# Kernel tuning notes

Hardware: AMD Instinct MI355X
Metric: run time of the kernel (lower is better)

Reference implementation:

```python
import jax, jax.numpy as jnp
import numpy as np

L = 32            # num_layers
R = 16            # lora_rank
P = L * 7         # 224 projections
D = 256           # encoder d_model
H = 4             # encoder heads
HD = D // H
FF = 2048         # TransformerEncoderLayer default dim_feedforward
PED = 512         # proj_embed_dim
HID = 4096
KV = 8 * (4096 // 32)   # 1024
INTER = 11008
VOCAB = 50000
NEG = -1e9

# projection index groups within the P=7*L ordering [q,k,v,o,gate,up,down]
IDX_A_HID = jnp.asarray((np.arange(L)[:, None] * 7 + np.array([0, 1, 2, 3, 4, 5])).reshape(-1))  # in_dim=4096
IDX_A_INT = jnp.asarray(np.arange(L) * 7 + 6)                                                    # in_dim=11008
IDX_B_HID = jnp.asarray((np.arange(L)[:, None] * 7 + np.array([0, 3, 6])).reshape(-1))           # out_dim=4096
IDX_B_KV  = jnp.asarray((np.arange(L)[:, None] * 7 + np.array([1, 2])).reshape(-1))              # out_dim=1024
IDX_B_INT = jnp.asarray((np.arange(L)[:, None] * 7 + np.array([4, 5])).reshape(-1))              # out_dim=11008


def _ln(x, g, b, eps=1e-5):
    m = jnp.mean(x, -1, keepdims=True)
    v = jnp.mean((x - m) ** 2, -1, keepdims=True)
    return (x - m) * jax.lax.rsqrt(v + eps) * g + b


def _enc_layer(x, pad, qw, qb, ow, ob, g1, b1, f1w, f1b, f2w, f2b, g2, b2):
    # post-norm TransformerEncoderLayer (torch default), relu FFN, eval mode (no dropout)
    Bsz, S, _ = x.shape
    qkv = x @ qw.T + qb                                  # [B,S,3D]
    q, k, v = jnp.split(qkv, 3, axis=-1)
    hd = lambda t: t.reshape(Bsz, S, H, HD).transpose(0, 2, 1, 3)
    q, k, v = hd(q), hd(k), hd(v)
    s = jnp.einsum('bhqd,bhkd->bhqk', q, k) / jnp.asarray(np.sqrt(HD), x.dtype)
    s = jnp.where(pad[:, None, None, :], NEG, s)
    a = jax.nn.softmax(s, -1)
    o = jnp.einsum('bhqk,bhkd->bhqd', a, v).transpose(0, 2, 1, 3).reshape(Bsz, S, D)
    x = _ln(x + o @ ow.T + ob, g1, b1)
    f = jax.nn.relu(x @ f1w.T + f1b) @ f2w.T + f2b
    return _ln(x + f, g2, b2)


def _forward(condition_ids, attention_mask, embed_table, enc_qkv_w, enc_qkv_b, enc_out_w, enc_out_b,
             enc_ln1_g, enc_ln1_b, enc_ff1_w, enc_ff1_b, enc_ff2_w, enc_ff2_b, enc_ln2_g, enc_ln2_b,
             proj_w, proj_b, a1_w, a1_b, a2_w, a2_b, b1_w, b1_b, b2_w, b2_b, scales):
    Bsz = condition_ids.shape[0]
    x = embed_table[condition_ids]                       # [B,S,256]
    pad = attention_mask == 0                            # key padding mask (~attention_mask)
    for l in range(3):
        x = _enc_layer(x, pad, enc_qkv_w[l], enc_qkv_b[l], enc_out_w[l], enc_out_b[l],
                       enc_ln1_g[l], enc_ln1_b[l], enc_ff1_w[l], enc_ff1_b[l],
                       enc_ff2_w[l], enc_ff2_b[l], enc_ln2_g[l], enc_ln2_b[l])
    am = attention_mask.astype(x.dtype)
    pooled = (x * am[..., None]).sum(1) / jnp.clip(am.sum(1, keepdims=True), 1.0)   # masked mean pool
    pe = (pooled @ proj_w.T + proj_b).reshape(Bsz, P, PED)                          # [B,224,512]

    def dec(w1, b1_, w2, b2_):
        return jax.nn.gelu(pe @ w1.T + b1_, approximate=False) @ w2.T + b2_

    A_base = dec(a1_w, a1_b, a2_w, a2_b).reshape(Bsz, P, R, 64)   # [B,P,r,64]
    B_base = dec(b1_w, b1_b, b2_w, b2_b).reshape(Bsz, P, 64, R)   # [B,P,64,r]
    sa, sb = scales[:, 0], scales[:, 1]

    def tile_A(idx, in_d):
        # all in_dims divisible by 64 => repeat(in_d//64+1)[:, :in_d] == exact tiling
        a = A_base[:, idx] * sa[idx][None, :, None, None]
        return jnp.tile(a, (1, 1, 1, in_d // 64))

    def tile_B(idx, out_d):
        b = B_base[:, idx] * sb[idx][None, :, None, None]
        return jnp.tile(b, (1, 1, out_d // 64, 1))

    return (tile_A(IDX_A_HID, HID), tile_A(IDX_A_INT, INTER),
            tile_B(IDX_B_HID, HID), tile_B(IDX_B_KV, KV), tile_B(IDX_B_INT, INTER))


def setup_inputs() -> dict:
    key = jax.random.key(0)
    ks = iter(jax.random.split(key, 40))
    rn = lambda shape, s=0.02: jax.random.normal(next(ks), shape, jnp.float32) * s
    Bsz, S = 4, 128
    return {
        'condition_ids': jax.random.randint(next(ks), (Bsz, S), 0, VOCAB),
        'attention_mask': jnp.ones((Bsz, S), jnp.int32),
        'embed_table': rn((VOCAB, D)),
        'enc_qkv_w': rn((3, 3 * D, D)), 'enc_qkv_b': rn((3, 3 * D)),
        'enc_out_w': rn((3, D, D)), 'enc_out_b': rn((3, D)),
        'enc_ln1_g': jnp.ones((3, D)), 'enc_ln1_b': jnp.zeros((3, D)),
        'enc_ff1_w': rn((3, FF, D)), 'enc_ff1_b': rn((3, FF)),
        'enc_ff2_w': rn((3, D, FF)), 'enc_ff2_b': rn((3, D)),
        'enc_ln2_g': jnp.ones((3, D)), 'enc_ln2_b': jnp.zeros((3, D)),
        'proj_w': rn((P * PED, D)), 'proj_b': rn((P * PED,)),
        'a1_w': rn((D, PED)), 'a1_b': rn((D,)),
        'a2_w': rn((R * 64, D)), 'a2_b': rn((R * 64,)),
        'b1_w': rn((D, PED)), 'b1_b': rn((D,)),
        'b2_w': rn((R * 64, D)), 'b2_b': rn((R * 64,)),
        'scales': jnp.full((P, 2), 0.01, jnp.float32),
    }


def reference(condition_ids, attention_mask, embed_table, enc_qkv_w, enc_qkv_b, enc_out_w, enc_out_b,
              enc_ln1_g, enc_ln1_b, enc_ff1_w, enc_ff1_b, enc_ff2_w, enc_ff2_b, enc_ln2_g, enc_ln2_b,
              proj_w, proj_b, a1_w, a1_b, a2_w, a2_b, b1_w, b1_b, b2_w, b2_b, scales):
    return _forward(condition_ids, attention_mask, embed_table, enc_qkv_w, enc_qkv_b, enc_out_w, enc_out_b,
                    enc_ln1_g, enc_ln1_b, enc_ff1_w, enc_ff1_b, enc_ff2_w, enc_ff2_b, enc_ln2_g, enc_ln2_b,
                    proj_w, proj_b, a1_w, a1_b, a2_w, a2_b, b1_w, b1_b, b2_w, b2_b, scales)
```

## Files before the change

### kernel.cpp

```cpp
#include <hip/hip_runtime.h>
#include <hip/hip_bf16.h>

typedef unsigned short u16;
typedef unsigned int u32;
typedef __attribute__((ext_vector_type(8))) short short8;
typedef __attribute__((ext_vector_type(4))) float floatx4;

__device__ __forceinline__ u16 f2bf(float f) {
  u32 x = __float_as_uint(f);
  x += 0x7FFFu + ((x >> 16) & 1u);
  return (u16)(x >> 16);
}
__device__ __forceinline__ u32 pk2(float lo, float hi) {
  return (u32)f2bf(lo) | ((u32)f2bf(hi) << 16);
}

__global__ void embed_kernel(const int* __restrict__ ids, const float* __restrict__ emb,
                             float* __restrict__ x) {
  int tok = blockIdx.x, d = threadIdx.x;
  x[tok * 256 + d] = emb[(size_t)ids[tok] * 256 + d];
}

template <int ACT, int SPLIT>
__global__ __launch_bounds__(256) void mfma_gemm_kernel(const float* __restrict__ A,
    const float* __restrict__ W, const float* __restrict__ bias, float* __restrict__ C,
    int M, int N, int K, int KS, int pstride) {
  __shared__ u16 Abf[64 * 32];
  __shared__ u16 Wbf[64 * 32];
  const int t = threadIdx.x;
  const int m0 = blockIdx.x * 64, n0 = blockIdx.y * 64;
  const int kz = blockIdx.z;
  const int srow = t >> 2, skc = (t & 3) * 8;
  const int w = t >> 6, lane = t & 63;
  const int q = lane >> 4, rr = lane & 15;
  floatx4 acc[4];
#pragma unroll
  for (int i = 0; i < 4; ++i) acc[i] = (floatx4){0.f, 0.f, 0.f, 0.f};

  const int kbeg = kz * KS, kend = kbeg + KS;
  for (int k0 = kbeg; k0 < kend; k0 += 32) {
    const float* ga = A + (size_t)(m0 + srow) * K + k0 + skc;
    const float* gw = W + (size_t)(n0 + srow) * K + k0 + skc;
    float4 a0 = *(const float4*)ga;
    float4 a1 = *(const float4*)(ga + 4);
    float4 w0 = *(const float4*)gw;
    float4 w1 = *(const float4*)(gw + 4);
    uint4 pa, pw;
    pa.x = pk2(a0.x, a0.y); pa.y = pk2(a0.z, a0.w);
    pa.z = pk2(a1.x, a1.y); pa.w = pk2(a1.z, a1.w);
    pw.x = pk2(w0.x, w0.y); pw.y = pk2(w0.z, w0.w);
    pw.z = pk2(w1.x, w1.y); pw.w = pk2(w1.z, w1.w);
    __syncthreads();
    *(uint4*)&Abf[srow * 32 + skc] = pa;
    *(uint4*)&Wbf[srow * 32 + skc] = pw;
    __syncthreads();
    short8 af = *(short8*)&Abf[(w * 16 + rr) * 32 + q * 8];
#pragma unroll
    for (int ct = 0; ct < 4; ++ct) {
      short8 bf = *(short8*)&Wbf[(ct * 16 + rr) * 32 + q * 8];
      acc[ct] = __builtin_amdgcn_mfma_f32_16x16x32_bf16(af, bf, acc[ct], 0, 0, 0);
    }
  }

  float* dst = SPLIT ? (C + (size_t)kz * pstride) : C;
#pragma unroll
  for (int ct = 0; ct < 4; ++ct) {
    int col = n0 + ct * 16 + rr;
#pragma unroll
    for (int r = 0; r < 4; ++r) {
      int row = m0 + w * 16 + q * 4 + r;
      float v = acc[ct][r];
      if (!SPLIT) {
        v += bias[col];
        if (ACT == 1) v = fmaxf(v, 0.f);
        if (ACT == 2) v = 0.5f * v * (1.f + erff(v * 0.70710678118654752f));
      }
      dst[(size_t)row * N + col] = v;
    }
  }
}

template <int ACT>
__global__ void red_bias_act_kernel(const float* __restrict__ parts, int nparts, int pstride,
                                    const float* __restrict__ bias, float* __restrict__ dst, int N) {
  int idx = blockIdx.x * 256 + threadIdx.x;
  float v = bias[idx % N];
  for (int p = 0; p < nparts; ++p) v += parts[(size_t)p * pstride + idx];
  if (ACT == 1) v = fmaxf(v, 0.f);
  if (ACT == 2) v = 0.5f * v * (1.f + erff(v * 0.70710678118654752f));
  dst[idx] = v;
}

__global__ __launch_bounds__(256) void attn_kernel(const float* __restrict__ qkv,
    const int* __restrict__ mask, float* __restrict__ o) {
  __shared__ float Klds[8192];
  __shared__ float Vlds[8192];
  const int blk = blockIdx.x;
  const int b = blk >> 7, h = (blk >> 5) & 3, qg = blk & 31;
  const int t = threadIdx.x;
  for (int i = t; i < 8192; i += 256) {
    int s = i >> 6, d = i & 63;
    size_t base = (size_t)(b * 128 + s) * 768 + h * 64 + d;
    Klds[(s << 6) + (d ^ (s & 31))] = qkv[base + 256];
    Vlds[i] = qkv[base + 512];
  }
  __syncthreads();
  const int wave = t >> 6, lane = t & 63;
  const int q = qg * 4 + wave;
  float qv = qkv[(size_t)(b * 128 + q) * 768 + h * 64 + lane];
  const int m0i = mask[b * 128 + lane];
  const int m1i = mask[b * 128 + 64 + lane];
  float s0 = 0.f, s1 = 0.f;
  const int sw = lane & 31;
  for (int d = 0; d < 64; ++d) {
    float qd = __shfl(qv, d);
    s0 += qd * Klds[(lane << 6) + (d ^ sw)];
    s1 += qd * Klds[((lane + 64) << 6) + (d ^ sw)];
  }
  s0 *= 0.125f; s1 *= 0.125f;
  if (m0i == 0) s0 = -1000000000.0f;
  if (m1i == 0) s1 = -1000000000.0f;
  float m = fmaxf(s0, s1);
  for (int off = 32; off; off >>= 1) m = fmaxf(m, __shfl_xor(m, off));
  float p0 = expf(s0 - m), p1 = expf(s1 - m);
  float sum = p0 + p1;
  for (int off = 32; off; off >>= 1) sum += __shfl_xor(sum, off);
  float rs = 1.f / sum;
  float acc = 0.f;
  for (int k = 0; k < 64; ++k) acc += __shfl(p0, k) * Vlds[(k << 6) + lane];
  for (int k = 0; k < 64; ++k) acc += __shfl(p1, k) * Vlds[((k + 64) << 6) + lane];
  o[(size_t)(b * 128 + q) * 256 + h * 64 + lane] = acc * rs;
}

__global__ __launch_bounds__(256) void add_ln_red_kernel(float* __restrict__ x,
    const float* __restrict__ parts, int nparts, int pstride, const float* __restrict__ bias,
    const float* __restrict__ g, const float* __restrict__ b) {
  int tok = blockIdx.x, t = threadIdx.x;
  int idx = tok * 256 + t;
  float r = x[idx] + bias[t];
  for (int p = 0; p < nparts; ++p) r += parts[(size_t)p * pstride + idx];
  float s = r, sq = r * r;
  for (int off = 32; off; off >>= 1) { s += __shfl_xor(s, off); sq += __shfl_xor(sq, off); }
  __shared__ float red[8];
  int wave = t >> 6, lane = t & 63;
  if (lane == 0) { red[wave] = s; red[4 + wave] = sq; }
  __syncthreads();
  float S = red[0] + red[1] + red[2] + red[3];
  float SQ = red[4] + red[5] + red[6] + red[7];
  float mean = S * (1.f / 256.f);
  float var = SQ * (1.f / 256.f) - mean * mean;
  float inv = 1.f / sqrtf(fmaxf(var, 0.f) + 1e-5f);
  x[idx] = (r - mean) * inv * g[t] + b[t];
}

__global__ void pool_kernel(const float* __restrict__ x, const int* __restrict__ mask,
                            float* __restrict__ pooled) {
  int b = blockIdx.x, d = threadIdx.x;
  float s = 0.f, c = 0.f;
  for (int ss = 0; ss < 128; ++ss) {
    float m = (float)mask[b * 128 + ss];
    s += m * x[(size_t)(b * 128 + ss) * 256 + d];
    c += m;
  }
  pooled[b * 256 + d] = s / fmaxf(c, 1.f);
}

__global__ __launch_bounds__(256) void proj_kernel(const float* __restrict__ pooled,
    const float* __restrict__ W, const float* __restrict__ bias, float* __restrict__ pe) {
  __shared__ float pl[1024];
  int t = threadIdx.x;
  for (int i = t; i < 1024; i += 256) pl[i] = pooled[i];
  __syncthreads();
  int wave = t >> 6, lane = t & 63;
  int half = lane >> 5, sl = lane & 31;
  int row = blockIdx.x * 8 + wave * 2 + half;
  float4 w0 = *(const float4*)(W + (size_t)row * 256 + sl * 8);
  float4 w1 = *(const float4*)(W + (size_t)row * 256 + sl * 8 + 4);
  float a0, a1, a2, a3;
#pragma unroll
  for (int bb = 0; bb < 4; ++bb) {
    const float* pp = &pl[bb * 256 + sl * 8];
    float v = w0.x * pp[0] + w0.y * pp[1] + w0.z * pp[2] + w0.w * pp[3]
            + w1.x * pp[4] + w1.y * pp[5] + w1.z * pp[6] + w1.w * pp[7];
    if (bb == 0) a0 = v; else if (bb == 1) a1 = v; else if (bb == 2) a2 = v; else a3 = v;
  }
#pragma unroll
  for (int off = 1; off < 32; off <<= 1) {
    a0 += __shfl_xor(a0, off); a1 += __shfl_xor(a1, off);
    a2 += __shfl_xor(a2, off); a3 += __shfl_xor(a3, off);
  }
  if (sl == 0) {
    float bv = bias[row];
    pe[0 * 114688 + row] = a0 + bv;
    pe[1 * 114688 + row] = a1 + bv;
    pe[2 * 114688 + row] = a2 + bv;
    pe[3 * 114688 + row] = a3 + bv;
  }
}

__global__ __launch_bounds__(256) void tile_a_kernel(const float* __restrict__ Abase,
    const float* __restrict__ scales, float* __restrict__ out, int nI, int ind,
    int pdiv, int pmul, int padd) {
  int row = blockIdx.x;
  int r = row & 15, bi = row >> 4;
  int i = bi % nI, b = bi / nI;
  int p = (i / pdiv) * 7 + (i % pdiv) * pmul + padd;
  float s = scales[2 * p];
  __shared__ float chunk[64];
  int t = threadIdx.x;
  if (t < 64) chunk[t] = Abase[((size_t)(b * 224 + p) * 16 + r) * 64 + t] * s;
  __syncthreads();
  size_t ob = (size_t)row * ind;
  for (int u = t; u * 4 < ind; u += 256) {
    int c0 = u * 4;
    float4 ov = *(const float4*)&chunk[c0 & 63];
    *(float4*)(out + ob + c0) = ov;
  }
}

__global__ __launch_bounds__(256) void tile_b_kernel(const float* __restrict__ Bbase,
    const float* __restrict__ scales, float* __restrict__ out, int nI, int ind, int nchunks,
    int pdiv, int pmul, int padd) {
  int blk = blockIdx.x;
  int cc = blk % nchunks, bi = blk / nchunks;
  int i = bi % nI, b = bi / nI;
  int p = (i / pdiv) * 7 + (i % pdiv) * pmul + padd;
  float s = scales[2 * p + 1];
  __shared__ float chunk[1024];
  int t = threadIdx.x;
  for (int e = t; e < 1024; e += 256) chunk[e] = Bbase[(size_t)(b * 224 + p) * 1024 + e] * s;
  __syncthreads();
  int cchunk16 = (ind / nchunks) * 16;
  size_t ob = (size_t)bi * ind * 16 + (size_t)cc * cchunk16;
  for (int u = t; u * 4 < cchunk16; u += 256) {
    int e0 = u * 4;
    int cabs = (cc * cchunk16 + e0) >> 4;
    int src = ((cabs & 63) << 4) + (e0 & 15);
    float4 ov = *(const float4*)&chunk[src];
    *(float4*)(out + ob + e0) = ov;
  }
}

extern "C" void kernel_launch(void* const* d_in, const int* in_sizes, int n_in,
                              void* d_out, int out_size, void* d_ws, size_t ws_size,
                              hipStream_t stream) {
  const int* ids     = (const int*)d_in[0];
  const int* mask    = (const int*)d_in[1];
  const float* emb   = (const float*)d_in[2];
  const float* qkv_w = (const float*)d_in[3];
  const float* qkv_b = (const float*)d_in[4];
  const float* out_w = (const float*)d_in[5];
  const float* out_b = (const float*)d_in[6];
  const float* ln1_g = (const float*)d_in[7];
  const float* ln1_b = (const float*)d_in[8];
  const float* ff1_w = (const float*)d_in[9];
  const float* ff1_b = (const float*)d_in[10];
  const float* ff2_w = (const float*)d_in[11];
  const float* ff2_b = (const float*)d_in[12];
  const float* ln2_g = (const float*)d_in[13];
  const float* ln2_b = (const float*)d_in[14];
  const float* proj_w = (const float*)d_in[15];
  const float* proj_b = (const float*)d_in[16];
  const float* a1_w = (const float*)d_in[17];
  const float* a1_b = (const float*)d_in[18];
  const float* a2_w = (const float*)d_in[19];
  const float* a2_b = (const float*)d_in[20];
  const float* b1_w = (const float*)d_in[21];
  const float* b1_b = (const float*)d_in[22];
  const float* b2_w = (const float*)d_in[23];
  const float* b2_b = (const float*)d_in[24];
  const float* scales = (const float*)d_in[25];

  float* w = (float*)d_ws;
  float* x      = w + 0;
  float* qkv    = w + 262144;
  float* attn_o = w + 655360;
  float* ff     = w + 786432;
  float* pooled = w + 1835008;
  float* pe     = w + 1836032;
  float* hA     = w + 2294784;
  float* hB     = w + 2524160;
  float* Abase  = w + 2753536;
  float* Bbase  = w + 3671040;
  float* parts  = w + 4588544;

  float* out = (float*)d_out;

  embed_kernel<<<512, 256, 0, stream>>>(ids, emb, x);
  for (int l = 0; l < 3; ++l) {
    mfma_gemm_kernel<0, 0><<<dim3(8, 12), 256, 0, stream>>>(
        x, qkv_w + l * 768 * 256, qkv_b + l * 768, qkv, 512, 768, 256, 256, 0);
    attn_kernel<<<512, 256, 0, stream>>>(qkv, mask, attn_o);
    mfma_gemm_kernel<0, 1><<<dim3(8, 4, 4), 256, 0, stream>>>(
        attn_o, out_w + l * 256 * 256, nullptr, parts, 512, 256, 256, 64, 131072);
    add_ln_red_kernel<<<512, 256, 0, stream>>>(x, parts, 4, 131072, out_b + l * 256,
                                               ln1_g + l * 256, ln1_b + l * 256);
    mfma_gemm_kernel<1, 0><<<dim3(8, 32), 256, 0, stream>>>(
        x, ff1_w + l * 2048 * 256, ff1_b + l * 2048, ff, 512, 2048, 256, 256, 0);
    mfma_gemm_kernel<0, 1><<<dim3(8, 4, 8), 256, 0, stream>>>(
        ff, ff2_w + l * 256 * 2048, nullptr, parts, 512, 256, 2048, 256, 131072);
    add_ln_red_kernel<<<512, 256, 0, stream>>>(x, parts, 8, 131072, ff2_b + l * 256,
                                               ln2_g + l * 256, ln2_b + l * 256);
  }
  pool_kernel<<<4, 256, 0, stream>>>(x, mask, pooled);
  proj_kernel<<<14336, 256, 0, stream>>>(pooled, proj_w, proj_b, pe);

  mfma_gemm_kernel<0, 1><<<dim3(14, 4, 4), 256, 0, stream>>>(
      pe, a1_w, nullptr, parts, 896, 256, 512, 128, 229376);
  red_bias_act_kernel<2><<<896, 256, 0, stream>>>(parts, 4, 229376, a1_b, hA, 256);
  mfma_gemm_kernel<0, 0><<<dim3(14, 16), 256, 0, stream>>>(
      hA, a2_w, a2_b, Abase, 896, 1024, 256, 256, 0);

  mfma_gemm_kernel<0, 1><<<dim3(14, 4, 4), 256, 0, stream>>>(
      pe, b1_w, nullptr, parts, 896, 256, 512, 128, 229376);
  red_bias_act_kernel<2><<<896, 256, 0, stream>>>(parts, 4, 229376, b1_b, hB, 256);
  mfma_gemm_kernel<0, 0><<<dim3(14, 16), 256, 0, stream>>>(
      hB, b2_w, b2_b, Bbase, 896, 1024, 256, 256, 0);

  tile_a_kernel<<<12288, 256, 0, stream>>>(Abase, scales, out, 192, 4096, 6, 1, 0);
  tile_a_kernel<<<2048, 256, 0, stream>>>(Abase, scales, out + 50331648ull, 32, 11008, 1, 0, 6);
  tile_b_kernel<<<3072, 256, 0, stream>>>(Bbase, scales, out + 72876032ull, 96, 4096, 8, 3, 3, 0);
  tile_b_kernel<<<512, 256, 0, stream>>>(Bbase, scales, out + 98041856ull, 64, 1024, 2, 2, 1, 1);
  tile_b_kernel<<<2048, 256, 0, stream>>>(Bbase, scales, out + 102236160ull, 64, 11008, 8, 2, 1, 4);
}
```

Baseline: 974.3 us.

## Fuse encoder layer stages into bf16 LDS-resident GEMM+LayerNorm kernels

```diff
diff --git a/kernel.cpp b/kernel.cpp
--- a/kernel.cpp
+++ b/kernel.cpp
@@ -11,14 +11,12 @@
   x += 0x7FFFu + ((x >> 16) & 1u);
   return (u16)(x >> 16);
 }
+__device__ __forceinline__ float bf2f(u16 u) { return __uint_as_float(((u32)u) << 16); }
 __device__ __forceinline__ u32 pk2(float lo, float hi) {
   return (u32)f2bf(lo) | ((u32)f2bf(hi) << 16);
 }
-
-__global__ void embed_kernel(const int* __restrict__ ids, const float* __restrict__ emb,
-                             float* __restrict__ x) {
-  int tok = blockIdx.x, d = threadIdx.x;
-  x[tok * 256 + d] = emb[(size_t)ids[tok] * 256 + d];
+__device__ __forceinline__ void mfma8(floatx4& acc, short8 a, short8 b) {
+  acc = __builtin_amdgcn_mfma_f32_16x16x32_bf16(a, b, acc, 0, 0, 0);
 }
 
 template <int ACT, int SPLIT>
@@ -36,7 +34,6 @@
   floatx4 acc[4];
 #pragma unroll
   for (int i = 0; i < 4; ++i) acc[i] = (floatx4){0.f, 0.f, 0.f, 0.f};
-
   const int kbeg = kz * KS, kend = kbeg + KS;
   for (int k0 = kbeg; k0 < kend; k0 += 32) {
     const float* ga = A + (size_t)(m0 + srow) * K + k0 + skc;
@@ -61,7 +58,6 @@
       acc[ct] = __builtin_amdgcn_mfma_f32_16x16x32_bf16(af, bf, acc[ct], 0, 0, 0);
     }
   }
-
   float* dst = SPLIT ? (C + (size_t)kz * pstride) : C;
 #pragma unroll
   for (int ct = 0; ct < 4; ++ct) {
@@ -80,19 +76,87 @@
   }
 }
 
-template <int ACT>
-__global__ void red_bias_act_kernel(const float* __restrict__ parts, int nparts, int pstride,
-                                    const float* __restrict__ bias, float* __restrict__ dst, int N) {
-  int idx = blockIdx.x * 256 + threadIdx.x;
-  float v = bias[idx % N];
-  for (int p = 0; p < nparts; ++p) v += parts[(size_t)p * pstride + idx];
-  if (ACT == 1) v = fmaxf(v, 0.f);
-  if (ACT == 2) v = 0.5f * v * (1.f + erff(v * 0.70710678118654752f));
-  dst[idx] = v;
-}
-
-__global__ __launch_bounds__(256) void attn_kernel(const float* __restrict__ qkv,
-    const int* __restrict__ mask, float* __restrict__ o) {
+struct WConvArgs {
+  const float* src[3];
+  u16* dst[3];
+  int cnt[3];
+};
+__global__ __launch_bounds__(256) void wconv_kernel(WConvArgs a) {
+  int tid = blockIdx.x * 256 + threadIdx.x;
+  int stride = gridDim.x * 256;
+  for (int s = 0; s < 3; ++s) {
+    const float* src = a.src[s];
+    u16* dst = a.dst[s];
+    int n4 = a.cnt[s] >> 2;
+    for (int i = tid; i < n4; i += stride) {
+      float4 v = ((const float4*)src)[i];
+      ushort4 o;
+      o.x = f2bf(v.x); o.y = f2bf(v.y); o.z = f2bf(v.z); o.w = f2bf(v.w);
+      ((ushort4*)dst)[i] = o;
+    }
+  }
+}
+
+template <int NB, int RELU, int BF16OUT>
+__device__ __forceinline__ void gemm_from_albs(const u16* Albs, u16* Wlds,
+    const u16* __restrict__ W, const float* __restrict__ bias, void* dst, int ldd,
+    int m0, int t, int w, int lane) {
+  const int rr = lane & 15, q = lane >> 4;
+  for (int nb = 0; nb < NB; ++nb) {
+#pragma unroll
+    for (int i = 0; i < 8; ++i) {
+      int idx = i * 256 + t, row = idx >> 5, col8 = (idx & 31) * 8;
+      *(uint4*)&Wlds[row * 264 + col8] = *(const uint4*)&W[(size_t)(nb * 64 + row) * 256 + col8];
+    }
+    __syncthreads();
+    floatx4 acc0 = (floatx4){0.f, 0.f, 0.f, 0.f};
+    floatx4 acc1 = (floatx4){0.f, 0.f, 0.f, 0.f};
+#pragma unroll
+    for (int k0 = 0; k0 < 256; k0 += 32) {
+      short8 a0 = *(const short8*)&Albs[rr * 264 + k0 + q * 8];
+      short8 a1 = *(const short8*)&Albs[(16 + rr) * 264 + k0 + q * 8];
+      short8 b = *(const short8*)&Wlds[(w * 16 + rr) * 264 + k0 + q * 8];
+      mfma8(acc0, a0, b);
+      mfma8(acc1, a1, b);
+    }
+    int col = nb * 64 + w * 16 + rr;
+    float bv = bias[col];
+#pragma unroll
+    for (int mt = 0; mt < 2; ++mt) {
+      floatx4 a = mt ? acc1 : acc0;
+#pragma unroll
+      for (int r = 0; r < 4; ++r) {
+        int row = m0 + mt * 16 + q * 4 + r;
+        float v = a[r] + bv;
+        if (RELU) v = fmaxf(v, 0.f);
+        if (BF16OUT)
+          ((u16*)dst)[(size_t)row * ldd + col] = f2bf(v);
+        else
+          ((float*)dst)[(size_t)row * ldd + col] = v;
+      }
+    }
+    __syncthreads();
+  }
+}
+
+__global__ __launch_bounds__(256) void embed_qkv_kernel(const int* __restrict__ ids,
+    const float* __restrict__ emb, float* __restrict__ x, const u16* __restrict__ qkvw,
+    const float* __restrict__ qkvb, u16* __restrict__ qkvbf) {
+  __shared__ u16 Albs[32 * 264];
+  __shared__ u16 Wlds[64 * 264];
+  const int t = threadIdx.x, w = t >> 6, lane = t & 63;
+  const int m0 = blockIdx.x * 32;
+  for (int r = 0; r < 32; ++r) {
+    float v = emb[(size_t)ids[m0 + r] * 256 + t];
+    x[(size_t)(m0 + r) * 256 + t] = v;
+    Albs[r * 264 + t] = f2bf(v);
+  }
+  __syncthreads();
+  gemm_from_albs<12, 0, 1>(Albs, Wlds, qkvw, qkvb, qkvbf, 768, m0, t, w, lane);
+}
+
+__global__ __launch_bounds__(256) void attn_kernel(const u16* __restrict__ qkv,
+    const int* __restrict__ mask, u16* __restrict__ o) {
   __shared__ float Klds[8192];
   __shared__ float Vlds[8192];
   const int blk = blockIdx.x;
@@ -101,13 +165,13 @@
   for (int i = t; i < 8192; i += 256) {
     int s = i >> 6, d = i & 63;
     size_t base = (size_t)(b * 128 + s) * 768 + h * 64 + d;
-    Klds[(s << 6) + (d ^ (s & 31))] = qkv[base + 256];
-    Vlds[i] = qkv[base + 512];
+    Klds[(s << 6) + (d ^ (s & 31))] = bf2f(qkv[base + 256]);
+    Vlds[i] = bf2f(qkv[base + 512]);
   }
   __syncthreads();
   const int wave = t >> 6, lane = t & 63;
   const int q = qg * 4 + wave;
-  float qv = qkv[(size_t)(b * 128 + q) * 768 + h * 64 + lane];
+  float qv = bf2f(qkv[(size_t)(b * 128 + q) * 768 + h * 64 + lane]);
   const int m0i = mask[b * 128 + lane];
   const int m1i = mask[b * 128 + 64 + lane];
   float s0 = 0.f, s1 = 0.f;
@@ -129,28 +193,128 @@
   float acc = 0.f;
   for (int k = 0; k < 64; ++k) acc += __shfl(p0, k) * Vlds[(k << 6) + lane];
   for (int k = 0; k < 64; ++k) acc += __shfl(p1, k) * Vlds[((k + 64) << 6) + lane];
-  o[(size_t)(b * 128 + q) * 256 + h * 64 + lane] = acc * rs;
-}
-
-__global__ __launch_bounds__(256) void add_ln_red_kernel(float* __restrict__ x,
-    const float* __restrict__ parts, int nparts, int pstride, const float* __restrict__ bias,
-    const float* __restrict__ g, const float* __restrict__ b) {
-  int tok = blockIdx.x, t = threadIdx.x;
-  int idx = tok * 256 + t;
-  float r = x[idx] + bias[t];
-  for (int p = 0; p < nparts; ++p) r += parts[(size_t)p * pstride + idx];
-  float s = r, sq = r * r;
-  for (int off = 32; off; off >>= 1) { s += __shfl_xor(s, off); sq += __shfl_xor(sq, off); }
-  __shared__ float red[8];
-  int wave = t >> 6, lane = t & 63;
-  if (lane == 0) { red[wave] = s; red[4 + wave] = sq; }
-  __syncthreads();
-  float S = red[0] + red[1] + red[2] + red[3];
-  float SQ = red[4] + red[5] + red[6] + red[7];
-  float mean = S * (1.f / 256.f);
-  float var = SQ * (1.f / 256.f) - mean * mean;
-  float inv = 1.f / sqrtf(fmaxf(var, 0.f) + 1e-5f);
-  x[idx] = (r - mean) * inv * g[t] + b[t];
+  o[(size_t)(b * 128 + q) * 256 + h * 64 + lane] = f2bf(acc * rs);
+}
+
+__global__ __launch_bounds__(256) void post1_kernel(float* __restrict__ x,
+    const u16* __restrict__ obf, const u16* __restrict__ outw, const float* __restrict__ outb,
+    const float* __restrict__ g1, const float* __restrict__ b1, const u16* __restrict__ ff1w,
+    const float* __restrict__ ff1b, float* __restrict__ ff) {
+  __shared__ u16 Albs[32 * 264];
+  __shared__ char ubuf[64 * 264 * 2];
+  u16* Wlds = (u16*)ubuf;
+  float* S = (float*)ubuf;
+  const int t = threadIdx.x, w = t >> 6, lane = t & 63;
+  const int rr = lane & 15, q = lane >> 4;
+  const int m0 = blockIdx.x * 32;
+#pragma unroll
+  for (int i = 0; i < 4; ++i) {
+    int idx = i * 256 + t, row = idx >> 5, col8 = (idx & 31) * 8;
+    *(uint4*)&Albs[row * 264 + col8] = *(const uint4*)&obf[(size_t)(m0 + row) * 256 + col8];
+  }
+  __syncthreads();
+  floatx4 accP[4][2];
+  for (int nb = 0; nb < 4; ++nb) {
+#pragma unroll
+    for (int i = 0; i < 8; ++i) {
+      int idx = i * 256 + t, row = idx >> 5, col8 = (idx & 31) * 8;
+      *(uint4*)&Wlds[row * 264 + col8] = *(const uint4*)&outw[(size_t)(nb * 64 + row) * 256 + col8];
+    }
+    __syncthreads();
+    floatx4 a0v = (floatx4){0.f, 0.f, 0.f, 0.f};
+    floatx4 a1v = (floatx4){0.f, 0.f, 0.f, 0.f};
+#pragma unroll
+    for (int k0 = 0; k0 < 256; k0 += 32) {
+      short8 a0 = *(const short8*)&Albs[rr * 264 + k0 + q * 8];
+      short8 a1 = *(const short8*)&Albs[(16 + rr) * 264 + k0 + q * 8];
+      short8 b = *(const short8*)&Wlds[(w * 16 + rr) * 264 + k0 + q * 8];
+      mfma8(a0v, a0, b);
+      mfma8(a1v, a1, b);
+    }
+    accP[nb][0] = a0v;
+    accP[nb][1] = a1v;
+    __syncthreads();
+  }
+#pragma unroll
+  for (int nb = 0; nb < 4; ++nb) {
+    int col = nb * 64 + w * 16 + rr;
+    float bv = outb[col];
+#pragma unroll
+    for (int mt = 0; mt < 2; ++mt)
+#pragma unroll
+      for (int r = 0; r < 4; ++r) {
+        int row = mt * 16 + q * 4 + r;
+        S[row * 264 + col] = accP[nb][mt][r] + bv + x[(size_t)(m0 + row) * 256 + col];
+      }
+  }
+  __syncthreads();
+  {
+    int j = t >> 3, s8 = t & 7;
+    float sm = 0.f, sq = 0.f;
+#pragma unroll
+    for (int ci = 0; ci < 32; ++ci) {
+      float v = S[j * 264 + ci * 8 + s8];
+      sm += v; sq += v * v;
+    }
+    for (int off = 1; off < 8; off <<= 1) { sm += __shfl_xor(sm, off); sq += __shfl_xor(sq, off); }
+    float mean = sm * (1.f / 256.f);
+    float var = sq * (1.f / 256.f) - mean * mean;
+    float inv = 1.f / sqrtf(fmaxf(var, 0.f) + 1e-5f);
+#pragma unroll
+    for (int ci = 0; ci < 32; ++ci) {
+      int col = ci * 8 + s8;
+      float v = (S[j * 264 + col] - mean) * inv * g1[col] + b1[col];
+      x[(size_t)(m0 + j) * 256 + col] = v;
+      Albs[j * 264 + col] = f2bf(v);
+    }
+  }
+  __syncthreads();
+  gemm_from_albs<32, 1, 0>(Albs, Wlds, ff1w, ff1b, ff, 2048, m0, t, w, lane);
+}
+
+template <int LAST>
+__global__ __launch_bounds__(256) void post2b_kernel(const float* __restrict__ parts,
+    const float* __restrict__ ff2b, const float* __restrict__ g2, const float* __restrict__ b2,
+    float* __restrict__ x, const u16* __restrict__ qkvw, const float* __restrict__ qkvb,
+    u16* __restrict__ qkvbf) {
+  __shared__ u16 Albs[32 * 264];
+  __shared__ char ubuf[64 * 264 * 2];
+  u16* Wlds = (u16*)ubuf;
+  float* S = (float*)ubuf;
+  const int t = threadIdx.x, w = t >> 6, lane = t & 63;
+  const int m0 = blockIdx.x * 32;
+  for (int e = t; e < 8192; e += 256) {
+    int row = e >> 8, col = e & 255;
+    size_t gi = (size_t)(m0 + row) * 256 + col;
+    float v = ff2b[col] + x[gi];
+#pragma unroll
+    for (int p = 0; p < 8; ++p) v += parts[(size_t)p * 131072 + gi];
+    S[row * 264 + col] = v;
+  }
+  __syncthreads();
+  {
+    int j = t >> 3, s8 = t & 7;
+    float sm = 0.f, sq = 0.f;
+#pragma unroll
+    for (int ci = 0; ci < 32; ++ci) {
+      float v = S[j * 264 + ci * 8 + s8];
+      sm += v; sq += v * v;
+    }
+    for (int off = 1; off < 8; off <<= 1) { sm += __shfl_xor(sm, off); sq += __shfl_xor(sq, off); }
+    float mean = sm * (1.f / 256.f);
+    float var = sq * (1.f / 256.f) - mean * mean;
+    float inv = 1.f / sqrtf(fmaxf(var, 0.f) + 1e-5f);
+#pragma unroll
+    for (int ci = 0; ci < 32; ++ci) {
+      int col = ci * 8 + s8;
+      float v = (S[j * 264 + col] - mean) * inv * g2[col] + b2[col];
+      x[(size_t)(m0 + j) * 256 + col] = v;
+      Albs[j * 264 + col] = f2bf(v);
+    }
+  }
+  __syncthreads();
+  if (!LAST)
+    gemm_from_albs<12, 0, 1>(Albs, Wlds, qkvw, qkvb, qkvbf, 768, m0, t, w, lane);
 }
 
 __global__ void pool_kernel(const float* __restrict__ x, const int* __restrict__ mask,
@@ -271,55 +435,68 @@
   const float* b2_b = (const float*)d_in[24];
   const float* scales = (const float*)d_in[25];
 
-  float* w = (float*)d_ws;
-  float* x      = w + 0;
-  float* qkv    = w + 262144;
-  float* attn_o = w + 655360;
-  float* ff     = w + 786432;
-  float* pooled = w + 1835008;
-  float* pe     = w + 1836032;
-  float* hA     = w + 2294784;
-  float* hB     = w + 2524160;
-  float* Abase  = w + 2753536;
-  float* Bbase  = w + 3671040;
-  float* parts  = w + 4588544;
+  u16* wb = (u16*)d_ws;
+  u16* qkvw_b = wb + 0;
+  u16* outw_b = wb + 589824;
+  u16* ff1w_b = wb + 786432;
+  u16* qkvbf  = wb + 2359296;
+  u16* obf    = wb + 2752512;
+  float* fw     = (float*)(wb + 2883584);
+  float* xbuf   = fw;
+  float* ff     = fw + 131072;
+  float* pooled = fw + 1179648;
+  float* pe     = fw + 1180672;
+  float* hA     = fw + 1639424;
+  float* hB     = fw + 1868800;
+  float* Abase  = fw + 2098176;
+  float* Bbase  = fw + 3015680;
+  float* parts  = fw + 3933184;
 
   float* out = (float*)d_out;
-
-  embed_kernel<<<512, 256, 0, stream>>>(ids, emb, x);
+  float* out0 = out;
+  float* out1 = out + 50331648ull;
+  float* out2 = out + 72876032ull;
+  float* out3 = out + 98041856ull;
+  float* out4 = out + 102236160ull;
+
+  WConvArgs wa;
+  wa.src[0] = qkv_w; wa.dst[0] = qkvw_b; wa.cnt[0] = 589824;
+  wa.src[1] = out_w; wa.dst[1] = outw_b; wa.cnt[1] = 196608;
+  wa.src[2] = ff1_w; wa.dst[2] = ff1w_b; wa.cnt[2] = 1572864;
+  wconv_kernel<<<512, 256, 0, stream>>>(wa);
+
+  embed_qkv_kernel<<<16, 256, 0, stream>>>(ids, emb, xbuf, qkvw_b, qkv_b, qkvbf);
   for (int l = 0; l < 3; ++l) {
-    mfma_gemm_kernel<0, 0><<<dim3(8, 12), 256, 0, stream>>>(
-        x, qkv_w + l * 768 * 256, qkv_b + l * 768, qkv, 512, 768, 256, 256, 0);
-    attn_kernel<<<512, 256, 0, stream>>>(qkv, mask, attn_o);
-    mfma_gemm_kernel<0, 1><<<dim3(8, 4, 4), 256, 0, stream>>>(
-        attn_o, out_w + l * 256 * 256, nullptr, parts, 512, 256, 256, 64, 131072);
-    add_ln_red_kernel<<<512, 256, 0, stream>>>(x, parts, 4, 131072, out_b + l * 256,
-                                               ln1_g + l * 256, ln1_b + l * 256);
-    mfma_gemm_kernel<1, 0><<<dim3(8, 32), 256, 0, stream>>>(
-        x, ff1_w + l * 2048 * 256, ff1_b + l * 2048, ff, 512, 2048, 256, 256, 0);
+    attn_kernel<<<512, 256, 0, stream>>>(qkvbf, mask, obf);
+    post1_kernel<<<16, 256, 0, stream>>>(xbuf, obf, outw_b + l * 65536, out_b + l * 256,
+                                         ln1_g + l * 256, ln1_b + l * 256,
+                                         ff1w_b + l * 524288, ff1_b + l * 2048, ff);
     mfma_gemm_kernel<0, 1><<<dim3(8, 4, 8), 256, 0, stream>>>(
-        ff, ff2_w + l * 256 * 2048, nullptr, parts, 512, 256, 2048, 256, 131072);
-    add_ln_red_kernel<<<512, 256, 0, stream>>>(x, parts, 8, 131072, ff2_b + l * 256,
-                                               ln2_g + l * 256, ln2_b + l * 256);
-  }
-  pool_kernel<<<4, 256, 0, stream>>>(x, mask, pooled);
+        ff, ff2_w + l * 524288, nullptr, parts, 512, 256, 2048, 256, 131072);
+    if (l < 2)
+      post2b_kernel<0><<<16, 256, 0, stream>>>(parts, ff2_b + l * 256, ln2_g + l * 256,
+                                               ln2_b + l * 256, xbuf,
+                                               qkvw_b + (l + 1) * 196608,
+                                               qkv_b + (l + 1) * 768, qkvbf);
+    else
+      post2b_kernel<1><<<16, 256, 0, stream>>>(parts, ff2_b + l * 256, ln2_g + l * 256,
+                                               ln2_b + l * 256, xbuf, qkvw_b, qkv_b, qkvbf);
+  }
+  pool_kernel<<<4, 256, 0, stream>>>(xbuf, mask, pooled);
   proj_kernel<<<14336, 256, 0, stream>>>(pooled, proj_w, proj_b, pe);
 
-  mfma_gemm_kernel<0, 1><<<dim3(14, 4, 4), 256, 0, stream>>>(
-      pe, a1_w, nullptr, parts, 896, 256, 512, 128, 229376);
-  red_bias_act_kernel<2><<<896, 256, 0, stream>>>(parts, 4, 229376, a1_b, hA, 256);
-  mfma_gemm_kernel<0, 0><<<dim3(14, 16), 256, 0, stream>>>(
-      hA, a2_w, a2_b, Abase, 896, 1024, 256, 256, 0);
-
-  mfma_gemm_kernel<0, 1><<<dim3(14, 4, 4), 256, 0, stream>>>(
-      pe, b1_w, nullptr, parts, 896, 256, 512, 128, 229376);
-  red_bias_act_kernel<2><<<896, 256, 0, stream>>>(parts, 4, 229376, b1_b, hB, 256);
-  mfma_gemm_kernel<0, 0><<<dim3(14, 16), 256, 0, stream>>>(
-      hB, b2_w, b2_b, Bbase, 896, 1024, 256, 256, 0);
-
-  tile_a_kernel<<<12288, 256, 0, stream>>>(Abase, scales, out, 192, 4096, 6, 1, 0);
-  tile_a_kernel<<<2048, 256, 0, stream>>>(Abase, scales, out + 50331648ull, 32, 11008, 1, 0, 6);
-  tile_b_kernel<<<3072, 256, 0, stream>>>(Bbase, scales, out + 72876032ull, 96, 4096, 8, 3, 3, 0);
-  tile_b_kernel<<<512, 256, 0, stream>>>(Bbase, scales, out + 98041856ull, 64, 1024, 2, 2, 1, 1);
-  tile_b_kernel<<<2048, 256, 0, stream>>>(Bbase, scales, out + 102236160ull, 64, 11008, 8, 2, 1, 4);
-}
+  mfma_gemm_kernel<2, 0><<<dim3(14, 4), 256, 0, stream>>>(pe, a1_w, a1_b, hA,
+                                                          896, 256, 512, 512, 0);
+  mfma_gemm_kernel<0, 0><<<dim3(14, 16), 256, 0, stream>>>(hA, a2_w, a2_b, Abase,
+                                                           896, 1024, 256, 256, 0);
+  mfma_gemm_kernel<2, 0><<<dim3(14, 4), 256, 0, stream>>>(pe, b1_w, b1_b, hB,
+                                                          896, 256, 512, 512, 0);
+  mfma_gemm_kernel<0, 0><<<dim3(14, 16), 256, 0, stream>>>(hB, b2_w, b2_b, Bbase,
+                                                           896, 1024, 256, 256, 0);
+
+  tile_a_kernel<<<12288, 256, 0, stream>>>(Abase, scales, out0, 192, 4096, 6, 1, 0);
+  tile_a_kernel<<<2048, 256, 0, stream>>>(Abase, scales, out1, 32, 11008, 1, 0, 6);
+  tile_b_kernel<<<3072, 256, 0, stream>>>(Bbase, scales, out2, 96, 4096, 8, 3, 3, 0);
+  tile_b_kernel<<<512, 256, 0, stream>>>(Bbase, scales, out3, 64, 1024, 2, 2, 1, 1);
+  tile_b_kernel<<<2048, 256, 0, stream>>>(Bbase, scales, out4, 64, 11008, 8, 2, 1, 4);
+}
```

Result: slower. 1.161 ms (+19.1%).
